# Kernel optimization log

Measured on AMD Instinct MI355X. Metric: run time of the kernel, lower is better.

The kernel has to match this reference:

```python
import jax, jax.numpy as jnp
import numpy as np

NEG = -10000.0
SLOPE = 0.2


def setup_inputs() -> dict:
    key = jax.random.key(0)
    k1, k2, k3, k4, k5 = jax.random.split(key, 5)
    B, N, F_in, F_out = 8, 2048, 512, 512
    text = jax.random.normal(k1, (B, N, F_in), dtype=jnp.float32)
    adj = jax.random.randint(k2, (B, N, N), 0, 2, dtype=jnp.int32)
    sc = 1.0 / np.sqrt(F_in)
    W = jax.random.normal(k3, (F_in, F_out), dtype=jnp.float32) * sc
    b = jnp.zeros((F_out,), dtype=jnp.float32)
    a_src = jax.random.normal(k4, (F_out,), dtype=jnp.float32) * sc
    a_dst = jax.random.normal(k5, (F_out,), dtype=jnp.float32) * sc
    return {"text": text, "adj": adj, "W": W, "b": b, "a_src": a_src, "a_dst": a_dst}


def reference(text, adj, W, b, a_src, a_dst):
    # hidden: [B, N, F_out]
    hidden = jnp.einsum("bnf,fo->bno", text, W) + b
    s = jnp.einsum("bno,o->bn", hidden, a_src)  # src score per node
    d = jnp.einsum("bno,o->bn", hidden, a_dst)  # dst score per node
    scores = s[:, :, None] + d[:, None, :]      # [B, N, N]
    scores = jnp.where(scores >= 0, scores, SLOPE * scores)  # LeakyReLU
    # faithful to original: masked_fill where adj.bool() is True
    scores = jnp.where(adj.astype(bool), NEG, scores)
    attn = jax.nn.softmax(scores, axis=-1)
    return jnp.einsum("bnm,bmo->bno", attn, hidden)
```

## Files before the change

### kernel.cpp

```cpp
#include <hip/hip_runtime.h>
#include <stdint.h>

#define NB 8
#define NN 2048
#define NF 512
#define TOTN (NB * NN)

typedef unsigned short u16;
typedef short bf16x8 __attribute__((ext_vector_type(8)));
typedef float f32x4 __attribute__((ext_vector_type(4)));

__device__ __forceinline__ u16 f2bf(float x) {
  unsigned u = __float_as_uint(x);
  unsigned r = 0x7FFFu + ((u >> 16) & 1u);
  return (u16)((u + r) >> 16);
}

__device__ __forceinline__ void gl2lds16(const void* g, void* l) {
  __builtin_amdgcn_global_load_lds((const __attribute__((address_space(1))) void*)g,
                                   (__attribute__((address_space(3))) void*)l,
                                   16, 0, 0);
}


__global__ __launch_bounds__(256) void conv_kernel(
    const float* __restrict__ text, const float* __restrict__ W,
    u16* __restrict__ text_bf, u16* __restrict__ Wt) {
  int blk = blockIdx.x;
  if (blk < 8192) {
    int idx = blk * 256 + threadIdx.x;
    float4 v = ((const float4*)text)[idx];
    ushort4 o;
    o.x = f2bf(v.x); o.y = f2bf(v.y); o.z = f2bf(v.z); o.w = f2bf(v.w);
    ((ushort4*)text_bf)[idx] = o;
  } else {
    int t = (blk - 8192) * 256 + threadIdx.x;
    int o = t >> 9, f = t & 511;
    Wt[o * NF + f] = f2bf(W[f * NF + o]);
  }
}

__global__ __launch_bounds__(256) void pack_kernel(
    const int* __restrict__ adj, uint32_t* __restrict__ bm) {
  int bid = blockIdx.x;
  int z = bid & 7, idx = bid >> 3;
  int gid = z * 131072 + idx * 256 + threadIdx.x;
  const int4* p = (const int4*)(adj + (size_t)gid * 32);
  uint32_t bits = 0;
#pragma unroll
  for (int c = 0; c < 8; ++c) {
    int4 a = p[c];
    bits |= (uint32_t)(a.x != 0) << (c * 4 + 0);
    bits |= (uint32_t)(a.y != 0) << (c * 4 + 1);
    bits |= (uint32_t)(a.z != 0) << (c * 4 + 2);
    bits |= (uint32_t)(a.w != 0) << (c * 4 + 3);
  }
  bm[gid] = bits;
}

__global__ __launch_bounds__(256) void gemm1_kernel(
    const u16* __restrict__ A,
    const u16* __restrict__ Bt,
    const float* __restrict__ bias, const float* __restrict__ a_src,
    const float* __restrict__ a_dst, u16* __restrict__ hS,
    float* __restrict__ s, float* __restrict__ d) {
  __shared__ u16 Alds[128 * 32];
  __shared__ u16 Blds[128 * 32];

  const int bid = blockIdx.x;
  const int zx = bid & 7, u = (bid >> 3) & 15, bm_ = bid >> 7;
  const int bn = zx * 16 + u;
  const int t = threadIdx.x, wave = t >> 6, lane = t & 63;
  const int wm = (wave >> 1) * 64, wn = (wave & 1) * 64;

  f32x4 acc[4][4];
#pragma unroll
  for (int i = 0; i < 4; ++i)
#pragma unroll
    for (int j = 0; j < 4; ++j) acc[i][j] = (f32x4){0.f, 0.f, 0.f, 0.f};

  const int rowA0 = bm_ * 128, rowB0 = bn * 128;
  const int srow = (lane >> 2);
  const int scol = (lane & 3) * 8;

  for (int kt = 0; kt < NF; kt += 32) {
#pragma unroll
    for (int q = 0; q < 2; ++q) {
      int r = wave * 32 + q * 16;
      gl2lds16(A + (size_t)(rowA0 + r + srow) * NF + (kt + scol), &Alds[r * 32]);
    }
#pragma unroll
    for (int q = 0; q < 2; ++q) {
      int r = wave * 32 + q * 16;
      gl2lds16(Bt + (size_t)(rowB0 + r + srow) * NF + (kt + scol), &Blds[r * 32]);
    }
    __syncthreads();

    const int fr = lane & 15;
    const int k0 = (lane >> 4) * 8;
    bf16x8 af[4], bfr[4];
#pragma unroll
    for (int i = 0; i < 4; ++i)
      af[i] = *(const bf16x8*)&Alds[(wm + i * 16 + fr) * 32 + k0];
#pragma unroll
    for (int j = 0; j < 4; ++j)
      bfr[j] = *(const bf16x8*)&Blds[(wn + j * 16 + fr) * 32 + k0];
#pragma unroll
    for (int i = 0; i < 4; ++i)
#pragma unroll
      for (int j = 0; j < 4; ++j)
        acc[i][j] = __builtin_amdgcn_mfma_f32_16x16x32_bf16(af[i], bfr[j],
                                                            acc[i][j], 0, 0, 0);
    __syncthreads();
  }

  const int quad = lane >> 4, ln16 = lane & 15;
  float sa[4] = {0.f, 0.f, 0.f, 0.f}, da[4] = {0.f, 0.f, 0.f, 0.f};
#pragma unroll
  for (int i = 0; i < 4; ++i) {
    int m0 = bm_ * 128 + wm + i * 16 + quad * 4;
#pragma unroll
    for (int r = 0; r < 4; ++r) {
      int m = m0 + r;
      float bv = bias[m];
      float asv = a_src[m], adv = a_dst[m];
      int oh = m >> 8, och = (m >> 4) & 15, rc = m & 15;
#pragma unroll
      for (int j = 0; j < 4; ++j) {
        int n = bn * 128 + wn + j * 16 + ln16;
        float h = acc[i][j][r] + bv;
        int zz = n >> 11, nz = n & 2047;
        int kc = nz >> 5, kin = nz & 31;
        size_t off = ((((size_t)zz * 2 + oh) * 64 + kc) << 13)
                     + (och << 9)
                     + ((size_t)(rc * 4 + ((kin >> 3) ^ ((rc >> 1) & 3))) << 3)
                     + (kin & 7);
        hS[off] = f2bf(h);
        sa[j] = fmaf(h, asv, sa[j]);
        da[j] = fmaf(h, adv, da[j]);
      }
    }
  }
#pragma unroll
  for (int j = 0; j < 4; ++j) {
    float v = sa[j] + __shfl_xor(sa[j], 16, 64);
    v += __shfl_xor(v, 32, 64);
    float w2 = da[j] + __shfl_xor(da[j], 16, 64);
    w2 += __shfl_xor(w2, 32, 64);
    if (quad == 0) {
      int n = bn * 128 + wn + j * 16 + ln16;
      atomicAdd(&s[n], v);
      atomicAdd(&d[n], w2);
    }
  }
}

__global__ __launch_bounds__(256, 2) void fused_attn_kernel(
    const uint32_t* __restrict__ bm, const float* __restrict__ s,
    const float* __restrict__ d, const u16* __restrict__ hS,
    float* __restrict__ out) {
  __shared__ u16 Blds[16384];
  __shared__ u16 Plds[4096];
  __shared__ float lpart[256];
  __shared__ float linv_lds[64];

  const int bid = blockIdx.x;
  const int z = bid & 7;
  const int rest = bid >> 3;
  const int oh = rest >> 5;
  const int i0 = (rest & 31) * 64;
  const int t = threadIdx.x, wave = t >> 6, lane = t & 63;
  const int quad = lane >> 4, ln16 = lane & 15;

  const int pr = t >> 2;
  const int ko = (t & 3) * 16;
  const float si = s[z * NN + i0 + pr];
  const uint32_t* bmrow = bm + (size_t)(z * NN + i0 + pr) * 64;
  const float* db = d + z * NN;

  const char* slabB = (const char*)hS + (size_t)(z * 2 + oh) * 1048576;

  f32x4 acc[4][4];
#pragma unroll
  for (int i = 0; i < 4; ++i)
#pragma unroll
    for (int j = 0; j < 4; ++j) acc[i][j] = (f32x4){0.f, 0.f, 0.f, 0.f};

  uint32_t bw = bmrow[ko >> 5];
  float4 dv[4];
#pragma unroll
  for (int c = 0; c < 4; ++c) dv[c] = *(const float4*)&db[ko + c * 4];

  const int fslot = ln16 * 4 + (quad ^ ((ln16 >> 1) & 3));
  const int prc = pr & 15, pch = pr >> 4;
  const int ph = ko >> 5, pq0 = (ko >> 3) & 3;
  char* pbase = (char*)Plds + ph * 4096 + pch * 1024;
  char* pdst0 = pbase + (prc * 4 + (pq0 ^ ((prc >> 1) & 3))) * 16;
  char* pdst1 = pbase + (prc * 4 + ((pq0 + 1) ^ ((prc >> 1) & 3))) * 16;

  float lsum = 0.f;

  for (int kt = 0; kt < NN; kt += 64) {
    uint32_t bits16 = (bw >> (ko & 16)) & 0xFFFFu;
    u16 pk[16];
#pragma unroll
    for (int cc = 0; cc < 4; ++cc) {
      float4 dq = dv[cc];
#pragma unroll
      for (int e = 0; e < 4; ++e) {
        float dj = (e == 0) ? dq.x : (e == 1) ? dq.y : (e == 2) ? dq.z : dq.w;
        float x = si + dj;
        float xm = fmaxf(x, 0.2f * x);
        float p = ((bits16 >> (cc * 4 + e)) & 1u) ? 0.f : __expf(xm);
        lsum += p;
        pk[cc * 4 + e] = f2bf(p);
      }
    }

    __syncthreads();

    *(int4*)pdst0 = *(int4*)&pk[0];
    *(int4*)pdst1 = *(int4*)&pk[8];

    {
      const char* gB = slabB + (size_t)kt * 512;
#pragma unroll
      for (int c = 0; c < 8; ++c) {
        int boff = (c * 4 + wave) * 1024;
        gl2lds16(gB + boff + lane * 16, (char*)Blds + boff);
      }
    }
    __syncthreads();

    if (kt + 64 < NN) {
      bw = bmrow[((kt + 64) >> 5) + (ko >> 5)];
#pragma unroll
      for (int c = 0; c < 4; ++c)
        dv[c] = *(const float4*)&db[kt + 64 + ko + c * 4];
    }

#pragma unroll
    for (int h = 0; h < 2; ++h) {
      bf16x8 af[4], bfv[4];
#pragma unroll
      for (int i = 0; i < 4; ++i)
        af[i] = *(const bf16x8*)((const char*)Plds + h * 4096 + i * 1024 + fslot * 16);
#pragma unroll
      for (int j = 0; j < 4; ++j)
        bfv[j] = *(const bf16x8*)((const char*)Blds + h * 16384 +
                                  (wave * 4 + j) * 1024 + fslot * 16);
#pragma unroll
      for (int i = 0; i < 4; ++i)
#pragma unroll
        for (int j = 0; j < 4; ++j)
          acc[i][j] = __builtin_amdgcn_mfma_f32_16x16x32_bf16(af[i], bfv[j],
                                                              acc[i][j], 0, 0, 0);
    }
  }

  lpart[pr * 4 + (t & 3)] = lsum;
  __syncthreads();
  if (t < 64) {
    const float* lp = &lpart[t * 4];
    linv_lds[t] = 1.0f / ((lp[0] + lp[1]) + (lp[2] + lp[3]));
  }
  __syncthreads();

#pragma unroll
  for (int i = 0; i < 4; ++i) {
#pragma unroll
    for (int r = 0; r < 4; ++r) {
      int m = i * 16 + quad * 4 + r;
      float sc = linv_lds[m];
      float* ob = out + ((size_t)(z * NN) + i0 + m) * NF + oh * 256 + wave * 64;
#pragma unroll
      for (int j = 0; j < 4; ++j) ob[j * 16 + ln16] = acc[i][j][r] * sc;
    }
  }
}

extern "C" void kernel_launch(void* const* d_in, const int* in_sizes, int n_in,
                              void* d_out, int out_size, void* d_ws,
                              size_t ws_size, hipStream_t stream) {
  const float* text  = (const float*)d_in[0];
  const int*   adj   = (const int*)d_in[1];
  const float* W     = (const float*)d_in[2];
  const float* bias  = (const float*)d_in[3];
  const float* a_src = (const float*)d_in[4];
  const float* a_dst = (const float*)d_in[5];
  float* out = (float*)d_out;

  char* ws = (char*)d_ws;
  u16*      text_bf = (u16*)(ws + 0);
  u16*      Wt      = (u16*)(ws + 16777216);
  u16*      hS      = (u16*)(ws + 17301504);
  float*    s       = (float*)(ws + 34078720);
  float*    d       = (float*)(ws + 34144256);
  uint32_t* bmask   = (uint32_t*)(ws + 34209792);

  hipMemsetAsync(s, 0, 131072, stream);

  conv_kernel<<<9216, 256, 0, stream>>>(text, W, text_bf, Wt);
  pack_kernel<<<4096, 256, 0, stream>>>(adj, bmask);

  gemm1_kernel<<<512, 256, 0, stream>>>(Wt, text_bf, bias, a_src, a_dst, hS, s, d);

  fused_attn_kernel<<<512, 256, 0, stream>>>(bmask, s, d, hS, out);
}
```

Before: 304.1 us.

## Load hidden B fragments directly from global in MFMA layout, widen attention block

The gemm1 epilogue now writes hidden in a per-lane MFMA fragment layout, so the attention kernel reads B operands straight from global/L2 into registers instead of staging them through LDS. The attention kernel uses 512-thread blocks covering all 512 output features, which halves the grid and removes the per-half recomputation of P. It also double-buffers the P tile in LDS so there is one barrier per iteration instead of two. The risk is that direct global loads expose more latency without LDS staging, and 256 blocks may underfill the GPU.

```diff
diff --git a/kernel.cpp b/kernel.cpp
--- a/kernel.cpp
+++ b/kernel.cpp
@@ -62,7 +62,7 @@
     const u16* __restrict__ A,
     const u16* __restrict__ Bt,
     const float* __restrict__ bias, const float* __restrict__ a_src,
-    const float* __restrict__ a_dst, u16* __restrict__ hS,
+    const float* __restrict__ a_dst, u16* __restrict__ Bg,
     float* __restrict__ s, float* __restrict__ d) {
   __shared__ u16 Alds[128 * 32];
   __shared__ u16 Blds[128 * 32];
@@ -124,18 +124,16 @@
       int m = m0 + r;
       float bv = bias[m];
       float asv = a_src[m], adv = a_dst[m];
-      int oh = m >> 8, och = (m >> 4) & 15, rc = m & 15;
+      int oc = m >> 4, oln = m & 15;
 #pragma unroll
       for (int j = 0; j < 4; ++j) {
         int n = bn * 128 + wn + j * 16 + ln16;
         float h = acc[i][j][r] + bv;
         int zz = n >> 11, nz = n & 2047;
-        int kc = nz >> 5, kin = nz & 31;
-        size_t off = ((((size_t)zz * 2 + oh) * 64 + kc) << 13)
-                     + (och << 9)
-                     + ((size_t)(rc * 4 + ((kin >> 3) ^ ((rc >> 1) & 3))) << 3)
-                     + (kin & 7);
-        hS[off] = f2bf(h);
+        int kc = nz >> 5, kq = (nz >> 3) & 3, ke = nz & 7;
+        size_t off = ((size_t)zz << 20) + (((size_t)kc * 32 + oc) << 9) +
+                     ((kq * 16 + oln) << 3) + ke;
+        Bg[off] = f2bf(h);
         sa[j] = fmaf(h, asv, sa[j]);
         da[j] = fmaf(h, adv, da[j]);
       }
@@ -155,30 +153,27 @@
   }
 }
 
-__global__ __launch_bounds__(256, 2) void fused_attn_kernel(
+__global__ __launch_bounds__(512, 2) void fused_attn_kernel(
     const uint32_t* __restrict__ bm, const float* __restrict__ s,
-    const float* __restrict__ d, const u16* __restrict__ hS,
+    const float* __restrict__ d, const u16* __restrict__ Bg,
     float* __restrict__ out) {
-  __shared__ u16 Blds[16384];
-  __shared__ u16 Plds[4096];
-  __shared__ float lpart[256];
+  __shared__ u16 Plds[2][4096];
+  __shared__ float lpart[512];
   __shared__ float linv_lds[64];
 
   const int bid = blockIdx.x;
   const int z = bid & 7;
-  const int rest = bid >> 3;
-  const int oh = rest >> 5;
-  const int i0 = (rest & 31) * 64;
+  const int i0 = (bid >> 3) * 64;
   const int t = threadIdx.x, wave = t >> 6, lane = t & 63;
   const int quad = lane >> 4, ln16 = lane & 15;
 
-  const int pr = t >> 2;
-  const int ko = (t & 3) * 16;
+  const int pr = t >> 3;
+  const int ko = (t & 7) * 8;
   const float si = s[z * NN + i0 + pr];
   const uint32_t* bmrow = bm + (size_t)(z * NN + i0 + pr) * 64;
   const float* db = d + z * NN;
 
-  const char* slabB = (const char*)hS + (size_t)(z * 2 + oh) * 1048576;
+  const u16* BgZ = Bg + ((size_t)z << 20);
 
   f32x4 acc[4][4];
 #pragma unroll
@@ -187,82 +182,76 @@
     for (int j = 0; j < 4; ++j) acc[i][j] = (f32x4){0.f, 0.f, 0.f, 0.f};
 
   uint32_t bw = bmrow[ko >> 5];
-  float4 dv[4];
-#pragma unroll
-  for (int c = 0; c < 4; ++c) dv[c] = *(const float4*)&db[ko + c * 4];
-
+  float4 dv0 = *(const float4*)&db[ko];
+  float4 dv1 = *(const float4*)&db[ko + 4];
+
+  const int prc = pr & 15, pch = pr >> 4;
+  const int ph = ko >> 5, pq = (ko >> 3) & 3;
+  const int pwoff = ph * 2048 + pch * 512 +
+                    (prc * 4 + (pq ^ ((prc >> 1) & 3))) * 8;
   const int fslot = ln16 * 4 + (quad ^ ((ln16 >> 1) & 3));
-  const int prc = pr & 15, pch = pr >> 4;
-  const int ph = ko >> 5, pq0 = (ko >> 3) & 3;
-  char* pbase = (char*)Plds + ph * 4096 + pch * 1024;
-  char* pdst0 = pbase + (prc * 4 + (pq0 ^ ((prc >> 1) & 3))) * 16;
-  char* pdst1 = pbase + (prc * 4 + ((pq0 + 1) ^ ((prc >> 1) & 3))) * 16;
 
   float lsum = 0.f;
-
-  for (int kt = 0; kt < NN; kt += 64) {
-    uint32_t bits16 = (bw >> (ko & 16)) & 0xFFFFu;
-    u16 pk[16];
-#pragma unroll
-    for (int cc = 0; cc < 4; ++cc) {
-      float4 dq = dv[cc];
-#pragma unroll
-      for (int e = 0; e < 4; ++e) {
-        float dj = (e == 0) ? dq.x : (e == 1) ? dq.y : (e == 2) ? dq.z : dq.w;
-        float x = si + dj;
-        float xm = fmaxf(x, 0.2f * x);
-        float p = ((bits16 >> (cc * 4 + e)) & 1u) ? 0.f : __expf(xm);
-        lsum += p;
-        pk[cc * 4 + e] = f2bf(p);
-      }
-    }
+  int par = 0;
+
+  for (int kt = 0; kt < NN; kt += 64, par ^= 1) {
+    uint32_t bits8 = (bw >> (ko & 31)) & 0xFFu;
+    float dva[8];
+    *(float4*)&dva[0] = dv0;
+    *(float4*)&dva[4] = dv1;
+    u16 pk[8];
+#pragma unroll
+    for (int e = 0; e < 8; ++e) {
+      float x = si + dva[e];
+      float xm = fmaxf(x, 0.2f * x);
+      float p = ((bits8 >> e) & 1u) ? 0.f : __expf(xm);
+      lsum += p;
+      pk[e] = f2bf(p);
+    }
+    *(int4*)((u16*)Plds + par * 4096 + pwoff) = *(int4*)pk;
 
     __syncthreads();
 
-    *(int4*)pdst0 = *(int4*)&pk[0];
-    *(int4*)pdst1 = *(int4*)&pk[8];
-
-    {
-      const char* gB = slabB + (size_t)kt * 512;
-#pragma unroll
-      for (int c = 0; c < 8; ++c) {
-        int boff = (c * 4 + wave) * 1024;
-        gl2lds16(gB + boff + lane * 16, (char*)Blds + boff);
-      }
-    }
-    __syncthreads();
+    const int kc0 = kt >> 5;
+    bf16x8 bfr[2][4];
+#pragma unroll
+    for (int h = 0; h < 2; ++h)
+#pragma unroll
+      for (int j = 0; j < 4; ++j)
+        bfr[h][j] = *(const bf16x8*)&BgZ[(((size_t)(kc0 + h) * 32 +
+                                           (wave * 4 + j)) << 9) + lane * 8];
 
     if (kt + 64 < NN) {
       bw = bmrow[((kt + 64) >> 5) + (ko >> 5)];
-#pragma unroll
-      for (int c = 0; c < 4; ++c)
-        dv[c] = *(const float4*)&db[kt + 64 + ko + c * 4];
-    }
-
-#pragma unroll
-    for (int h = 0; h < 2; ++h) {
-      bf16x8 af[4], bfv[4];
+      dv0 = *(const float4*)&db[kt + 64 + ko];
+      dv1 = *(const float4*)&db[kt + 64 + ko + 4];
+    }
+
+    bf16x8 af[2][4];
+#pragma unroll
+    for (int h = 0; h < 2; ++h)
 #pragma unroll
       for (int i = 0; i < 4; ++i)
-        af[i] = *(const bf16x8*)((const char*)Plds + h * 4096 + i * 1024 + fslot * 16);
-#pragma unroll
-      for (int j = 0; j < 4; ++j)
-        bfv[j] = *(const bf16x8*)((const char*)Blds + h * 16384 +
-                                  (wave * 4 + j) * 1024 + fslot * 16);
+        af[h][i] = *(const bf16x8*)((const u16*)Plds + par * 4096 + h * 2048 +
+                                    i * 512 + fslot * 8);
+#pragma unroll
+    for (int h = 0; h < 2; ++h)
 #pragma unroll
       for (int i = 0; i < 4; ++i)
 #pragma unroll
         for (int j = 0; j < 4; ++j)
-          acc[i][j] = __builtin_amdgcn_mfma_f32_16x16x32_bf16(af[i], bfv[j],
+          acc[i][j] = __builtin_amdgcn_mfma_f32_16x16x32_bf16(af[h][i],
+                                                              bfr[h][j],
                                                               acc[i][j], 0, 0, 0);
-    }
-  }
-
-  lpart[pr * 4 + (t & 3)] = lsum;
+  }
+
+  lpart[pr * 8 + (t & 7)] = lsum;
   __syncthreads();
   if (t < 64) {
-    const float* lp = &lpart[t * 4];
-    linv_lds[t] = 1.0f / ((lp[0] + lp[1]) + (lp[2] + lp[3]));
+    const float* lp = &lpart[t * 8];
+    float tot = ((lp[0] + lp[1]) + (lp[2] + lp[3])) +
+                ((lp[4] + lp[5]) + (lp[6] + lp[7]));
+    linv_lds[t] = 1.0f / tot;
   }
   __syncthreads();
 
@@ -272,7 +261,7 @@
     for (int r = 0; r < 4; ++r) {
       int m = i * 16 + quad * 4 + r;
       float sc = linv_lds[m];
-      float* ob = out + ((size_t)(z * NN) + i0 + m) * NF + oh * 256 + wave * 64;
+      float* ob = out + ((size_t)(z * NN) + i0 + m) * NF + wave * 64;
 #pragma unroll
       for (int j = 0; j < 4; ++j) ob[j * 16 + ln16] = acc[i][j][r] * sc;
     }
@@ -293,7 +282,7 @@
   char* ws = (char*)d_ws;
   u16*      text_bf = (u16*)(ws + 0);
   u16*      Wt      = (u16*)(ws + 16777216);
-  u16*      hS      = (u16*)(ws + 17301504);
+  u16*      Bg      = (u16*)(ws + 17301504);
   float*    s       = (float*)(ws + 34078720);
   float*    d       = (float*)(ws + 34144256);
   uint32_t* bmask   = (uint32_t*)(ws + 34209792);
@@ -303,7 +292,7 @@
   conv_kernel<<<9216, 256, 0, stream>>>(text, W, text_bf, Wt);
   pack_kernel<<<4096, 256, 0, stream>>>(adj, bmask);
 
-  gemm1_kernel<<<512, 256, 0, stream>>>(Wt, text_bf, bias, a_src, a_dst, hS, s, d);
-
-  fused_attn_kernel<<<512, 256, 0, stream>>>(bmask, s, d, hS, out);
-}
+  gemm1_kernel<<<512, 256, 0, stream>>>(Wt, text_bf, bias, a_src, a_dst, Bg, s, d);
+
+  fused_attn_kernel<<<256, 512, 0, stream>>>(bmask, s, d, Bg, out);
+}
```

Result: no change. 303.5 us (-0.2%).
